# Kernel tuning notes

Hardware: AMD Instinct MI355X
Metric: run time of the kernel (lower is better)

The kernel has to match this reference:

```python
import jax, jax.numpy as jnp
import numpy as np
from math import factorial

# ---- static config mirroring Cace.__init__ ----
MAX_L = 3            # max angular degree
N_RBF = 8            # Bessel radial basis size
RB = 8               # n_radial_basis (radial embedding dim after transform)
K = 3                # n_atom_basis -> edge channels C = K*K
NZ = 4               # len(zs)
CUTOFF = 5.5
N_NODES = 2000
N_EDGES = 50000
T_MP = 1             # num_message_passing
MP_NORM = 1.0 / np.sqrt(25.0)   # 1/sqrt(avg_num_neighbors)
C = K * K

def _lxlylz(max_l):
    out = []
    for l in range(max_l + 1):
        for lx in range(l, -1, -1):
            for ly in range(l - lx, -1, -1):
                out.append((lx, ly, l - lx - ly))
    return out

L_LIST = _lxlylz(MAX_L)                 # 20 Cartesian monomials for max_l=3
NL = len(L_LIST)
LX = np.array([t[0] for t in L_LIST]); LY = np.array([t[1] for t in L_LIST]); LZ = np.array([t[2] for t in L_LIST])
DEGS = LX + LY + LZ                     # degree l of each monomial
MULTI = np.array([factorial(int(d)) / (factorial(int(a)) * factorial(int(b)) * factorial(int(c)))
                  for a, b, c, d in zip(LX, LY, LZ, DEGS)], dtype=np.float32)
SEL = np.zeros((NL, MAX_L + 1), np.float32)
SEL[np.arange(NL), DEGS] = 1.0          # monomial -> degree one-hot (for per-l sums)
NB = 1 + (MAX_L + 1)                    # symmetrizer feats: nu=1 (l=0) + nu=2 per l

def bessel(r):  # [E] -> [E, N_RBF]
    n = jnp.arange(1, N_RBF + 1, dtype=r.dtype)
    return jnp.sqrt(2.0 / CUTOFF) * jnp.sin(n[None, :] * jnp.pi * r[:, None] / CUTOFF) / r[:, None]

def poly_cutoff(r):  # MACE-style polynomial cutoff, p=6
    p = 6.0
    u = r / CUTOFF
    f = 1.0 - (p + 1.0) * (p + 2.0) / 2.0 * u**6 + p * (p + 2.0) * u**7 - p * (p + 1.0) / 2.0 * u**8
    return f * (u < 1.0)

def axis_pows(x):  # [E] -> [E, MAX_L+1] = x^0..x^MAX_L (safe grads, handles negatives)
    pows = [jnp.ones_like(x)]
    for _ in range(MAX_L):
        pows.append(pows[-1] * x)
    return jnp.stack(pows, axis=1)

def angular(u):  # unit vectors [E,3] -> Cartesian monomials [E, NL]
    return axis_pows(u[:, 0])[:, LX] * axis_pows(u[:, 1])[:, LY] * axis_pows(u[:, 2])[:, LZ]

def radial_transform(x, W):  # x [N,R,L,C], W [MAX_L+1,R,Rb] shared per degree l
    return jnp.einsum('nrlc,lrb->nblc', x, W[DEGS])

def symmetrize(A):  # A [N,Rb,NL,C] -> B [N,Rb,NB,C]
    b1 = A[:, :, :1, :]  # nu=1: the (0,0,0) monomial (index 0)
    w = (A * A) * jnp.asarray(MULTI)[None, None, :, None]
    b2 = jnp.einsum('nrlc,lm->nrmc', w, jnp.asarray(SEL))  # nu=2 invariant per degree l
    return jnp.concatenate([b1, b2], axis=2)


def setup_inputs() -> dict:
    key = jax.random.key(0)
    ks = jax.random.split(key, 9)
    positions = jax.random.uniform(ks[0], (N_NODES, 3), dtype=jnp.float32) * 12.0
    species = jax.random.randint(ks[1], (N_NODES,), 0, NZ)
    send = jax.random.randint(ks[2], (N_EDGES,), 0, N_NODES)
    off = jax.random.randint(ks[3], (N_EDGES,), 1, N_NODES)
    recv = (send + off) % N_NODES  # no self-edges -> strictly positive edge lengths
    edge_index = jnp.stack([send, recv])
    shifts = jnp.zeros((N_EDGES, 3), jnp.float32)
    W_embed = jax.random.normal(ks[4], (NZ, K), jnp.float32)
    W_radial = jax.random.normal(ks[5], (MAX_L + 1, N_RBF, RB), jnp.float32) / np.sqrt(N_RBF)
    W_mem = jax.random.normal(ks[6], (MAX_L + 1, RB, RB), jnp.float32) / np.sqrt(RB)
    W_ar = jax.random.normal(ks[7], (N_RBF, RB), jnp.float32) / np.sqrt(N_RBF)
    W_chi = jax.random.normal(ks[8], (RB, NB), jnp.float32) * 0.1
    return {"positions": positions, "shifts": shifts, "W_embed": W_embed, "W_radial": W_radial,
            "W_mem": W_mem, "W_ar": W_ar, "W_chi": W_chi, "species": species, "edge_index": edge_index}


def reference(positions, shifts, W_embed, W_radial, W_mem, W_ar, W_chi, species, edge_index):
    n_nodes = positions.shape[0]
    send, recv = edge_index[0], edge_index[1]
    # edge geometry
    vec = positions[recv] - positions[send] + shifts
    lengths = jnp.linalg.norm(vec, axis=-1)
    u = vec / (lengths[:, None] + 1e-9)
    rad = bessel(lengths)          # [E,R]
    fcut = poly_cutoff(lengths)    # [E]
    ang = angular(u)               # [E,NL]
    # edge type encoding: outer product of sender/receiver species embeddings
    emb = W_embed[species]         # [N,K]
    enc = (emb[send][:, :, None] * emb[recv][:, None, :]).reshape(-1, C)  # [E,C]
    # elementwise_multiply_3tensors -> [E,R,NL,C]
    edge_attri = jnp.einsum('er,el,ec->erlc', rad * fcut[:, None], ang, enc)
    A = radial_transform(jax.ops.segment_sum(edge_attri, recv, num_segments=n_nodes), W_radial)  # [N,Rb,NL,C]
    B = symmetrize(A)              # [N,Rb,NB,C]
    feats = [B]
    for _ in range(T_MP):
        mem = jnp.einsum('nrlc,lrb->nblc', A, W_mem[DEGS])        # NodeMemory
        chi = jnp.einsum('nbkc,bk->nc', B, W_chi)                  # MessageBchi node scalar
        msg_bchi = edge_attri * chi[send][:, None, None, :]
        A_bchi = radial_transform(jax.ops.segment_sum(msg_bchi, recv, num_segments=n_nodes), W_radial)
        fr = (rad @ W_ar) * fcut[:, None]                          # MessageAr radial filter [E,Rb]
        msg_ar = A[send] * fr[:, :, None, None]
        A_ar = jax.ops.segment_sum(msg_ar, recv, num_segments=n_nodes)
        A = (A_ar + A_bchi) * MP_NORM + mem
        B = symmetrize(A)
        feats.append(B)
    return jnp.stack(feats, axis=-1)   # [N,Rb,NB,C,T_MP+1]
```

## Files before the change

### kernel.cpp

```cpp
#include <hip/hip_runtime.h>
#include <hip/hip_bf16.h>


#define CUTF 5.5f
#define MPNORM 0.2f

__constant__ int   d_DEGS[20]  = {0,1,1,1,2,2,2,2,2,2,3,3,3,3,3,3,3,3,3,3};
__constant__ float d_MULTI[20] = {1,1,1,1,1,2,2,1,2,1,1,3,3,3,6,3,1,3,3,1};

__global__ void k_count(const int* __restrict__ eidx, int* __restrict__ counts, int E) {
  int e = blockIdx.x * blockDim.x + threadIdx.x;
  if (e < E) atomicAdd(&counts[eidx[E + e]], 1);
}

__global__ void k_scan(const int* __restrict__ counts, int* __restrict__ offs, int N) {
  __shared__ int part[256];
  int t = threadIdx.x;
  int local[8]; int sum = 0;
  #pragma unroll
  for (int i = 0; i < 8; i++) {
    int idx = t*8 + i;
    int v = (idx < N) ? counts[idx] : 0;
    local[i] = sum; sum += v;
  }
  part[t] = sum; __syncthreads();
  for (int d = 1; d < 256; d <<= 1) {
    int add = (t >= d) ? part[t-d] : 0;
    __syncthreads();
    part[t] += add;
    __syncthreads();
  }
  int excl = part[t] - sum;
  #pragma unroll
  for (int i = 0; i < 8; i++) {
    int idx = t*8 + i;
    if (idx < N) offs[idx] = excl + local[i];
  }
  if (t == 255) offs[N] = part[255];
}

__global__ void k_edge(const float* __restrict__ pos,
                       const float* __restrict__ shifts,
                       const float* __restrict__ Wemb,
                       const float* __restrict__ War,
                       const int* __restrict__ species,
                       const int* __restrict__ eidx,
                       const int* __restrict__ offs,
                       int* __restrict__ cursor,
                       float* __restrict__ edata,
                       int* __restrict__ esend,
                       int E) {
  __shared__ float war_s[64];
  int t = threadIdx.x;
  if (t < 64) war_s[t] = War[t];
  __syncthreads();
  int e = blockIdx.x * blockDim.x + t;
  if (e >= E) return;
  int s  = eidx[e];
  int rI = eidx[E + e];
  float vx = pos[rI*3+0] - pos[s*3+0] + shifts[e*3+0];
  float vy = pos[rI*3+1] - pos[s*3+1] + shifts[e*3+1];
  float vz = pos[rI*3+2] - pos[s*3+2] + shifts[e*3+2];
  float len = sqrtf(vx*vx + vy*vy + vz*vz);
  float inv = 1.0f / (len + 1e-9f);
  float ux = vx*inv, uy = vy*inv, uz = vz*inv;
  float uu = len * (1.0f/CUTF);
  float u2 = uu*uu, u6 = u2*u2*u2;
  float fcut = (uu < 1.0f) ? (1.0f - 28.0f*u6 + 48.0f*u6*uu - 21.0f*u6*u2) : 0.0f;
  float x = 3.14159265358979f * uu;
  float sn = sinf(x), c2 = 2.0f*cosf(x), snm1 = 0.0f;
  float pref = sqrtf(2.0f/CUTF) / (len + 1e-20f);
  float rad[8];
  float v[48];
  #pragma unroll
  for (int k = 0; k < 8; k++) {
    rad[k] = pref * sn;
    v[k]   = rad[k] * fcut;
    float nxt = c2*sn - snm1; snm1 = sn; sn = nxt;
  }
  #pragma unroll
  for (int b = 0; b < 8; b++) {
    float a = 0.0f;
    #pragma unroll
    for (int k = 0; k < 8; k++) a += rad[k] * war_s[k*8+b];
    v[8+b] = a * fcut;
  }
  float px2 = ux*ux, py2 = uy*uy, pz2 = uz*uz;
  v[16] = 1.0f; v[17] = ux;     v[18] = uy;     v[19] = uz;
  v[20] = px2;  v[21] = ux*uy;  v[22] = ux*uz;  v[23] = py2;
  v[24] = uy*uz;v[25] = pz2;
  v[26] = px2*ux; v[27] = px2*uy; v[28] = px2*uz; v[29] = ux*py2;
  v[30] = ux*uy*uz; v[31] = ux*pz2; v[32] = py2*uy; v[33] = py2*uz;
  v[34] = uy*pz2; v[35] = pz2*uz;
  int zs = species[s], zr = species[rI];
  float es0 = Wemb[zs*3+0], es1 = Wemb[zs*3+1], es2 = Wemb[zs*3+2];
  float er0 = Wemb[zr*3+0], er1 = Wemb[zr*3+1], er2 = Wemb[zr*3+2];
  v[36] = es0*er0; v[37] = es0*er1; v[38] = es0*er2;
  v[39] = es1*er0; v[40] = es1*er1; v[41] = es1*er2;
  v[42] = es2*er0; v[43] = es2*er1; v[44] = es2*er2;
  v[45] = 0.0f; v[46] = 0.0f; v[47] = 0.0f;
  int slot = atomicAdd(&cursor[rI], 1);
  int dst = offs[rI] + slot;
  float4* eb4 = reinterpret_cast<float4*>(edata + (size_t)dst * 48);
  #pragma unroll
  for (int w = 0; w < 12; w++)
    eb4[w] = make_float4(v[4*w], v[4*w+1], v[4*w+2], v[4*w+3]);
  esend[dst] = s;
}

__global__ __launch_bounds__(192) void k_nodeA(
    const float* __restrict__ edata, const int* __restrict__ offs,
    const float* __restrict__ Wrad, const float* __restrict__ Wchi,
    float* __restrict__ A, unsigned int* __restrict__ Abf2,
    float* __restrict__ chi, float* __restrict__ B0, int N) {
  __shared__ float wr_s[288];
  __shared__ float wchi_s[40];
  __shared__ float Bsh[360];
  int t = threadIdx.x, n = blockIdx.x;
  for (int i = t; i < 256; i += 192) { int d = i >> 6, rm = i & 63; wr_s[d*72+rm] = Wrad[i]; }
  for (int i = t; i < 40;  i += 192) wchi_s[i] = Wchi[i];
  for (int i = t; i < 360; i += 192) Bsh[i] = 0.0f;
  int l = t / 9, c = t - l*9;
  bool act = t < 180;
  int ll = act ? l : 0, cc = act ? c : 0;
  float acc[8];
  #pragma unroll
  for (int r = 0; r < 8; r++) acc[r] = 0.0f;
  int start = offs[n], end = offs[n+1];
  #pragma unroll 4
  for (int j = start; j < end; j++) {
    const float* row = edata + (size_t)j * 48;
    float p = row[16+ll] * row[36+cc];
    #pragma unroll
    for (int r = 0; r < 8; r++) acc[r] += row[r] * p;
  }
  __syncthreads();
  int deg = act ? d_DEGS[ll] : 0;
  const float* wp = &wr_s[deg*72];
  float Ab[8];
  #pragma unroll
  for (int b = 0; b < 8; b++) {
    float a = 0.0f;
    #pragma unroll
    for (int r = 0; r < 8; r++) a += acc[r] * wp[r*8+b];
    Ab[b] = a;
  }
  if (act) {
    #pragma unroll
    for (int b = 0; b < 8; b++) A[(size_t)n*1440 + t*8 + b] = Ab[b];
    #pragma unroll
    for (int bp = 0; bp < 4; bp++) {
      __hip_bfloat16 blo = __float2bfloat16(Ab[2*bp]);
      __hip_bfloat16 bhi = __float2bfloat16(Ab[2*bp+1]);
      unsigned int pr = (unsigned int)(*reinterpret_cast<unsigned short*>(&blo))
                      | ((unsigned int)(*reinterpret_cast<unsigned short*>(&bhi)) << 16);
      Abf2[(size_t)bp*N*180 + (size_t)n*180 + t] = pr;
    }
    if (l == 0) {
      #pragma unroll
      for (int b = 0; b < 8; b++) Bsh[b*45 + c] = Ab[b];
    }
    float mlt = d_MULTI[ll]; int kk = 1 + deg;
    #pragma unroll
    for (int b = 0; b < 8; b++) atomicAdd(&Bsh[b*45 + kk*9 + c], mlt*Ab[b]*Ab[b]);
  }
  __syncthreads();
  if (t < 9) {
    float s = 0.0f;
    for (int b = 0; b < 8; b++)
      #pragma unroll
      for (int kq = 0; kq < 5; kq++) s += Bsh[b*45 + kq*9 + t] * wchi_s[b*5 + kq];
    chi[n*9 + t] = s;
  }
  for (int i = t; i < 360; i += 192)
    B0[(size_t)n*360 + i] = Bsh[i];
}

__global__ __launch_bounds__(192) void k_node2(
    const float* __restrict__ edata, const int* __restrict__ esend,
    const int* __restrict__ offs,
    const float* __restrict__ Wrad, const float* __restrict__ Wmem,
    const float* __restrict__ A, const unsigned int* __restrict__ Abf2,
    const float* __restrict__ chi, const float* __restrict__ B0,
    float* __restrict__ out, int N) {
  __shared__ float wr_s[288], wm_s[288];
  __shared__ float Bsh[360];
  int t = threadIdx.x, n = blockIdx.x;
  for (int i = t; i < 256; i += 192) {
    int d = i >> 6, rm = i & 63;
    wr_s[d*72+rm] = Wrad[i];
    wm_s[d*72+rm] = Wmem[i];
  }
  for (int i = t; i < 360; i += 192) Bsh[i] = 0.0f;
  int l = t / 9, c = t - l*9;
  bool act = t < 180;
  int ll = act ? l : 0, cc = act ? c : 0;
  int tt = act ? t : 0;
  size_t plane = (size_t)N * 180;
  float Sacc[8], ARacc[8];
  #pragma unroll
  for (int r = 0; r < 8; r++) { Sacc[r] = 0.0f; ARacc[r] = 0.0f; }
  int start = offs[n], end = offs[n+1];
  #pragma unroll 4
  for (int j = start; j < end; j++) {
    const float* row = edata + (size_t)j * 48;
    int snd = esend[j];
    float ch = chi[snd*9 + cc];
    float pch = row[16+ll] * row[36+cc] * ch;
    #pragma unroll
    for (int r = 0; r < 8; r++) Sacc[r] += row[r] * pch;
    const unsigned int* gp = Abf2 + (size_t)snd*180 + tt;
    unsigned int q0 = gp[0];
    unsigned int q1 = gp[plane];
    unsigned int q2 = gp[2*plane];
    unsigned int q3 = gp[3*plane];
    float a0 = __uint_as_float(q0 << 16), a1 = __uint_as_float(q0 & 0xffff0000u);
    float a2 = __uint_as_float(q1 << 16), a3 = __uint_as_float(q1 & 0xffff0000u);
    float a4 = __uint_as_float(q2 << 16), a5 = __uint_as_float(q2 & 0xffff0000u);
    float a6 = __uint_as_float(q3 << 16), a7 = __uint_as_float(q3 & 0xffff0000u);
    ARacc[0] += a0*row[8];  ARacc[1] += a1*row[9];
    ARacc[2] += a2*row[10]; ARacc[3] += a3*row[11];
    ARacc[4] += a4*row[12]; ARacc[5] += a5*row[13];
    ARacc[6] += a6*row[14]; ARacc[7] += a7*row[15];
  }
  __syncthreads();
  if (act) {
    int deg = d_DEGS[ll];
    const float* wrp = &wr_s[deg*72];
    const float* wmp = &wm_s[deg*72];
    const float* aop = A + (size_t)n*1440 + t*8;
    float aown[8];
    #pragma unroll
    for (int r = 0; r < 8; r++) aown[r] = aop[r];
    float newA[8];
    #pragma unroll
    for (int b = 0; b < 8; b++) {
      float mem = 0.0f, ab = 0.0f;
      #pragma unroll
      for (int r = 0; r < 8; r++) { mem += aown[r]*wmp[r*8+b]; ab += Sacc[r]*wrp[r*8+b]; }
      newA[b] = (ARacc[b] + ab)*MPNORM + mem;
    }
    if (l == 0) {
      #pragma unroll
      for (int b = 0; b < 8; b++) Bsh[b*45 + c] = newA[b];
    }
    float mlt = d_MULTI[ll]; int kk = 1 + deg;
    #pragma unroll
    for (int b = 0; b < 8; b++) atomicAdd(&Bsh[b*45 + kk*9 + c], mlt*newA[b]*newA[b]);
  }
  __syncthreads();
  float2* out2 = reinterpret_cast<float2*>(out);
  for (int i = t; i < 360; i += 192) {
    float2 pk; pk.x = B0[(size_t)n*360 + i]; pk.y = Bsh[i];
    out2[(size_t)n*360 + i] = pk;
  }
}

extern "C" void kernel_launch(void* const* d_in, const int* in_sizes, int n_in,
                              void* d_out, int out_size, void* d_ws, size_t ws_size,
                              hipStream_t stream) {
  const float* pos    = (const float*)d_in[0];
  const float* shifts = (const float*)d_in[1];
  const float* Wemb   = (const float*)d_in[2];
  const float* Wrad   = (const float*)d_in[3];
  const float* Wmem   = (const float*)d_in[4];
  const float* War    = (const float*)d_in[5];
  const float* Wchi   = (const float*)d_in[6];
  const int* species = (const int*)d_in[7];
  const int* eidx    = (const int*)d_in[8];
  float* out = (float*)d_out;
  int N = in_sizes[7];
  int E = in_sizes[8] / 2;

  char* base = (char*)d_ws;
  size_t off = 0;
  float* edata = (float*)(base + off); off += (size_t)E*48*4;
  float* A     = (float*)(base + off); off += (size_t)N*1440*4;
  unsigned int* Abf2 = (unsigned int*)(base + off); off += (size_t)N*180*4*4;
  float* chi   = (float*)(base + off); off += (size_t)N*9*4;
  float* B0    = (float*)(base + off); off += (size_t)N*360*4;
  int* counts  = (int*)(base + off);   off += (size_t)N*4;
  int* cursor  = (int*)(base + off);   off += (size_t)N*4;
  int* offs    = (int*)(base + off);   off += (((size_t)(N+1)*4) + 15) & ~(size_t)15;
  int* esend   = (int*)(base + off);   off += (size_t)E*4;

  hipMemsetAsync(counts, 0, (size_t)N*2*4, stream);
  int eb = (E + 255) / 256;
  k_count<<<eb, 256, 0, stream>>>(eidx, counts, E);
  k_scan<<<1, 256, 0, stream>>>(counts, offs, N);
  k_edge<<<eb, 256, 0, stream>>>(pos, shifts, Wemb, War, species, eidx, offs, cursor,
                                 edata, esend, E);
  k_nodeA<<<N, 192, 0, stream>>>(edata, offs, Wrad, Wchi, A, Abf2, chi, B0, N);
  k_node2<<<N, 192, 0, stream>>>(edata, esend, offs, Wrad, Wmem, A, Abf2, chi, B0, out, N);
}
```

Baseline: 169.2 us.

## Reuse count-atomic ranks, vectorize bf16 A gather, split and prefetch edge loops

k_count now records each edge's slot from its counting atomic, so k_edge no longer needs a second atomic pass over a cursor array or its memset. The packed bf16 copy of A changes from four strided planes to one uint4 per thread, so each neighbour gather is a single 16-byte load. Both node kernels split each node's edge list into two halves with separate accumulators to expose more independent loads. k_node2 also prefetches the next sender's A and chi values one step ahead. k_edge moves to 64-thread blocks. The cost is more registers in the node kernels, which can lower occupancy, and a small change in summation order.

Result: faster. 154.9 us (-8.4%).

```diff
diff --git a/kernel.cpp b/kernel.cpp
--- a/kernel.cpp
+++ b/kernel.cpp
@@ -8,9 +8,10 @@
 __constant__ int   d_DEGS[20]  = {0,1,1,1,2,2,2,2,2,2,3,3,3,3,3,3,3,3,3,3};
 __constant__ float d_MULTI[20] = {1,1,1,1,1,2,2,1,2,1,1,3,3,3,6,3,1,3,3,1};
 
-__global__ void k_count(const int* __restrict__ eidx, int* __restrict__ counts, int E) {
+__global__ void k_count(const int* __restrict__ eidx, int* __restrict__ counts,
+                        int* __restrict__ erank, int E) {
   int e = blockIdx.x * blockDim.x + threadIdx.x;
-  if (e < E) atomicAdd(&counts[eidx[E + e]], 1);
+  if (e < E) erank[e] = atomicAdd(&counts[eidx[E + e]], 1);
 }
 
 __global__ void k_scan(const int* __restrict__ counts, int* __restrict__ offs, int N) {
@@ -39,25 +40,27 @@
   if (t == 255) offs[N] = part[255];
 }
 
-__global__ void k_edge(const float* __restrict__ pos,
+__global__ __launch_bounds__(64) void k_edge(
+                       const float* __restrict__ pos,
                        const float* __restrict__ shifts,
                        const float* __restrict__ Wemb,
                        const float* __restrict__ War,
                        const int* __restrict__ species,
                        const int* __restrict__ eidx,
                        const int* __restrict__ offs,
-                       int* __restrict__ cursor,
+                       const int* __restrict__ erank,
                        float* __restrict__ edata,
                        int* __restrict__ esend,
                        int E) {
   __shared__ float war_s[64];
   int t = threadIdx.x;
-  if (t < 64) war_s[t] = War[t];
-  __syncthreads();
-  int e = blockIdx.x * blockDim.x + t;
+  war_s[t] = War[t];
+  __syncthreads();
+  int e = blockIdx.x * 64 + t;
   if (e >= E) return;
   int s  = eidx[e];
   int rI = eidx[E + e];
+  int rk = erank[e];
   float vx = pos[rI*3+0] - pos[s*3+0] + shifts[e*3+0];
   float vy = pos[rI*3+1] - pos[s*3+1] + shifts[e*3+1];
   float vz = pos[rI*3+2] - pos[s*3+2] + shifts[e*3+2];
@@ -99,8 +102,7 @@
   v[39] = es1*er0; v[40] = es1*er1; v[41] = es1*er2;
   v[42] = es2*er0; v[43] = es2*er1; v[44] = es2*er2;
   v[45] = 0.0f; v[46] = 0.0f; v[47] = 0.0f;
-  int slot = atomicAdd(&cursor[rI], 1);
-  int dst = offs[rI] + slot;
+  int dst = offs[rI] + rk;
   float4* eb4 = reinterpret_cast<float4*>(edata + (size_t)dst * 48);
   #pragma unroll
   for (int w = 0; w < 12; w++)
@@ -111,7 +113,7 @@
 __global__ __launch_bounds__(192) void k_nodeA(
     const float* __restrict__ edata, const int* __restrict__ offs,
     const float* __restrict__ Wrad, const float* __restrict__ Wchi,
-    float* __restrict__ A, unsigned int* __restrict__ Abf2,
+    float* __restrict__ A, uint4* __restrict__ Abf2,
     float* __restrict__ chi, float* __restrict__ B0, int N) {
   __shared__ float wr_s[288];
   __shared__ float wchi_s[40];
@@ -123,17 +125,31 @@
   int l = t / 9, c = t - l*9;
   bool act = t < 180;
   int ll = act ? l : 0, cc = act ? c : 0;
+  int s0 = offs[n], e0 = offs[n+1];
+  int len = e0 - s0;
+  int half = len >> 1;
+  int mid = s0 + half;
+  float accA[8], accB[8];
+  #pragma unroll
+  for (int r = 0; r < 8; r++) { accA[r] = 0.0f; accB[r] = 0.0f; }
+  #pragma unroll 2
+  for (int i = 0; i < half; i++) {
+    const float* rA = edata + (size_t)(s0 + i) * 48;
+    const float* rB = edata + (size_t)(mid + i) * 48;
+    float pA = rA[16+ll] * rA[36+cc];
+    float pB = rB[16+ll] * rB[36+cc];
+    #pragma unroll
+    for (int r = 0; r < 8; r++) { accA[r] += rA[r] * pA; accB[r] += rB[r] * pB; }
+  }
+  if (len & 1) {
+    const float* rA = edata + (size_t)(e0 - 1) * 48;
+    float pA = rA[16+ll] * rA[36+cc];
+    #pragma unroll
+    for (int r = 0; r < 8; r++) accA[r] += rA[r] * pA;
+  }
   float acc[8];
   #pragma unroll
-  for (int r = 0; r < 8; r++) acc[r] = 0.0f;
-  int start = offs[n], end = offs[n+1];
-  #pragma unroll 4
-  for (int j = start; j < end; j++) {
-    const float* row = edata + (size_t)j * 48;
-    float p = row[16+ll] * row[36+cc];
-    #pragma unroll
-    for (int r = 0; r < 8; r++) acc[r] += row[r] * p;
-  }
+  for (int r = 0; r < 8; r++) acc[r] = accA[r] + accB[r];
   __syncthreads();
   int deg = act ? d_DEGS[ll] : 0;
   const float* wp = &wr_s[deg*72];
@@ -148,14 +164,16 @@
   if (act) {
     #pragma unroll
     for (int b = 0; b < 8; b++) A[(size_t)n*1440 + t*8 + b] = Ab[b];
+    unsigned int pk[4];
     #pragma unroll
     for (int bp = 0; bp < 4; bp++) {
       __hip_bfloat16 blo = __float2bfloat16(Ab[2*bp]);
       __hip_bfloat16 bhi = __float2bfloat16(Ab[2*bp+1]);
-      unsigned int pr = (unsigned int)(*reinterpret_cast<unsigned short*>(&blo))
-                      | ((unsigned int)(*reinterpret_cast<unsigned short*>(&bhi)) << 16);
-      Abf2[(size_t)bp*N*180 + (size_t)n*180 + t] = pr;
-    }
+      pk[bp] = (unsigned int)(*reinterpret_cast<unsigned short*>(&blo))
+             | ((unsigned int)(*reinterpret_cast<unsigned short*>(&bhi)) << 16);
+    }
+    uint4 qv; qv.x = pk[0]; qv.y = pk[1]; qv.z = pk[2]; qv.w = pk[3];
+    Abf2[(size_t)n*180 + t] = qv;
     if (l == 0) {
       #pragma unroll
       for (int b = 0; b < 8; b++) Bsh[b*45 + c] = Ab[b];
@@ -180,7 +198,7 @@
     const float* __restrict__ edata, const int* __restrict__ esend,
     const int* __restrict__ offs,
     const float* __restrict__ Wrad, const float* __restrict__ Wmem,
-    const float* __restrict__ A, const unsigned int* __restrict__ Abf2,
+    const float* __restrict__ A, const uint4* __restrict__ Abf2,
     const float* __restrict__ chi, const float* __restrict__ B0,
     float* __restrict__ out, int N) {
   __shared__ float wr_s[288], wm_s[288];
@@ -196,33 +214,72 @@
   bool act = t < 180;
   int ll = act ? l : 0, cc = act ? c : 0;
   int tt = act ? t : 0;
-  size_t plane = (size_t)N * 180;
+  int s0 = offs[n], e0 = offs[n+1];
+  int len = e0 - s0;
+  int half = len >> 1;
+  int mid = s0 + half;
+  float SA[8], SB[8], RA[8], RB[8];
+  #pragma unroll
+  for (int r = 0; r < 8; r++) { SA[r]=0.0f; SB[r]=0.0f; RA[r]=0.0f; RB[r]=0.0f; }
+  uint4 qA, qB; float chA, chB;
+  if (half > 0) {
+    int sA = esend[s0], sB = esend[mid];
+    qA  = Abf2[(size_t)sA*180 + tt];
+    qB  = Abf2[(size_t)sB*180 + tt];
+    chA = chi[sA*9 + cc];
+    chB = chi[sB*9 + cc];
+  }
+  for (int i = 0; i < half; i++) {
+    uint4 nqA, nqB; float nchA, nchB;
+    bool more = (i + 1 < half);
+    if (more) {
+      int sA = esend[s0 + i + 1], sB = esend[mid + i + 1];
+      nqA  = Abf2[(size_t)sA*180 + tt];
+      nqB  = Abf2[(size_t)sB*180 + tt];
+      nchA = chi[sA*9 + cc];
+      nchB = chi[sB*9 + cc];
+    }
+    const float* rA = edata + (size_t)(s0 + i) * 48;
+    const float* rB = edata + (size_t)(mid + i) * 48;
+    float pA = rA[16+ll] * rA[36+cc];
+    float pB = rB[16+ll] * rB[36+cc];
+    float pcA = pA * chA, pcB = pB * chB;
+    #pragma unroll
+    for (int r = 0; r < 8; r++) { SA[r] += rA[r] * pcA; SB[r] += rB[r] * pcB; }
+    float a0 = __uint_as_float(qA.x << 16), a1 = __uint_as_float(qA.x & 0xffff0000u);
+    float a2 = __uint_as_float(qA.y << 16), a3 = __uint_as_float(qA.y & 0xffff0000u);
+    float a4 = __uint_as_float(qA.z << 16), a5 = __uint_as_float(qA.z & 0xffff0000u);
+    float a6 = __uint_as_float(qA.w << 16), a7 = __uint_as_float(qA.w & 0xffff0000u);
+    RA[0] += a0*rA[8];  RA[1] += a1*rA[9];  RA[2] += a2*rA[10]; RA[3] += a3*rA[11];
+    RA[4] += a4*rA[12]; RA[5] += a5*rA[13]; RA[6] += a6*rA[14]; RA[7] += a7*rA[15];
+    float b0 = __uint_as_float(qB.x << 16), b1 = __uint_as_float(qB.x & 0xffff0000u);
+    float b2 = __uint_as_float(qB.y << 16), b3 = __uint_as_float(qB.y & 0xffff0000u);
+    float b4 = __uint_as_float(qB.z << 16), b5 = __uint_as_float(qB.z & 0xffff0000u);
+    float b6 = __uint_as_float(qB.w << 16), b7 = __uint_as_float(qB.w & 0xffff0000u);
+    RB[0] += b0*rB[8];  RB[1] += b1*rB[9];  RB[2] += b2*rB[10]; RB[3] += b3*rB[11];
+    RB[4] += b4*rB[12]; RB[5] += b5*rB[13]; RB[6] += b6*rB[14]; RB[7] += b7*rB[15];
+    if (more) { qA = nqA; chA = nchA; qB = nqB; chB = nchB; }
+  }
+  if (len & 1) {
+    int j = e0 - 1;
+    int sA = esend[j];
+    const uint4 qT = Abf2[(size_t)sA*180 + tt];
+    float chT = chi[sA*9 + cc];
+    const float* rA = edata + (size_t)j * 48;
+    float pA = rA[16+ll] * rA[36+cc];
+    float pcA = pA * chT;
+    #pragma unroll
+    for (int r = 0; r < 8; r++) SA[r] += rA[r] * pcA;
+    float a0 = __uint_as_float(qT.x << 16), a1 = __uint_as_float(qT.x & 0xffff0000u);
+    float a2 = __uint_as_float(qT.y << 16), a3 = __uint_as_float(qT.y & 0xffff0000u);
+    float a4 = __uint_as_float(qT.z << 16), a5 = __uint_as_float(qT.z & 0xffff0000u);
+    float a6 = __uint_as_float(qT.w << 16), a7 = __uint_as_float(qT.w & 0xffff0000u);
+    RA[0] += a0*rA[8];  RA[1] += a1*rA[9];  RA[2] += a2*rA[10]; RA[3] += a3*rA[11];
+    RA[4] += a4*rA[12]; RA[5] += a5*rA[13]; RA[6] += a6*rA[14]; RA[7] += a7*rA[15];
+  }
   float Sacc[8], ARacc[8];
   #pragma unroll
-  for (int r = 0; r < 8; r++) { Sacc[r] = 0.0f; ARacc[r] = 0.0f; }
-  int start = offs[n], end = offs[n+1];
-  #pragma unroll 4
-  for (int j = start; j < end; j++) {
-    const float* row = edata + (size_t)j * 48;
-    int snd = esend[j];
-    float ch = chi[snd*9 + cc];
-    float pch = row[16+ll] * row[36+cc] * ch;
-    #pragma unroll
-    for (int r = 0; r < 8; r++) Sacc[r] += row[r] * pch;
-    const unsigned int* gp = Abf2 + (size_t)snd*180 + tt;
-    unsigned int q0 = gp[0];
-    unsigned int q1 = gp[plane];
-    unsigned int q2 = gp[2*plane];
-    unsigned int q3 = gp[3*plane];
-    float a0 = __uint_as_float(q0 << 16), a1 = __uint_as_float(q0 & 0xffff0000u);
-    float a2 = __uint_as_float(q1 << 16), a3 = __uint_as_float(q1 & 0xffff0000u);
-    float a4 = __uint_as_float(q2 << 16), a5 = __uint_as_float(q2 & 0xffff0000u);
-    float a6 = __uint_as_float(q3 << 16), a7 = __uint_as_float(q3 & 0xffff0000u);
-    ARacc[0] += a0*row[8];  ARacc[1] += a1*row[9];
-    ARacc[2] += a2*row[10]; ARacc[3] += a3*row[11];
-    ARacc[4] += a4*row[12]; ARacc[5] += a5*row[13];
-    ARacc[6] += a6*row[14]; ARacc[7] += a7*row[15];
-  }
+  for (int r = 0; r < 8; r++) { Sacc[r] = SA[r] + SB[r]; ARacc[r] = RA[r] + RB[r]; }
   __syncthreads();
   if (act) {
     int deg = d_DEGS[ll];
@@ -276,20 +333,19 @@
   size_t off = 0;
   float* edata = (float*)(base + off); off += (size_t)E*48*4;
   float* A     = (float*)(base + off); off += (size_t)N*1440*4;
-  unsigned int* Abf2 = (unsigned int*)(base + off); off += (size_t)N*180*4*4;
+  uint4* Abf2  = (uint4*)(base + off); off += (size_t)N*180*16;
   float* chi   = (float*)(base + off); off += (size_t)N*9*4;
   float* B0    = (float*)(base + off); off += (size_t)N*360*4;
   int* counts  = (int*)(base + off);   off += (size_t)N*4;
-  int* cursor  = (int*)(base + off);   off += (size_t)N*4;
   int* offs    = (int*)(base + off);   off += (((size_t)(N+1)*4) + 15) & ~(size_t)15;
   int* esend   = (int*)(base + off);   off += (size_t)E*4;
-
-  hipMemsetAsync(counts, 0, (size_t)N*2*4, stream);
-  int eb = (E + 255) / 256;
-  k_count<<<eb, 256, 0, stream>>>(eidx, counts, E);
+  int* erank   = (int*)(base + off);   off += (((size_t)E*4) + 15) & ~(size_t)15;
+
+  hipMemsetAsync(counts, 0, (size_t)N*4, stream);
+  k_count<<<(E + 255) / 256, 256, 0, stream>>>(eidx, counts, erank, E);
   k_scan<<<1, 256, 0, stream>>>(counts, offs, N);
-  k_edge<<<eb, 256, 0, stream>>>(pos, shifts, Wemb, War, species, eidx, offs, cursor,
-                                 edata, esend, E);
+  k_edge<<<(E + 63) / 64, 64, 0, stream>>>(pos, shifts, Wemb, War, species, eidx,
+                                           offs, erank, edata, esend, E);
   k_nodeA<<<N, 192, 0, stream>>>(edata, offs, Wrad, Wchi, A, Abf2, chi, B0, N);
   k_node2<<<N, 192, 0, stream>>>(edata, esend, offs, Wrad, Wmem, A, Abf2, chi, B0, out, N);
 }
```
